# Kernel tuning notes

Measured on AMD Instinct MI355X. Metric: run time of the kernel, lower is better.

The kernel has to match this reference:

```python
import jax, jax.numpy as jnp
import numpy as np

N_NODES = 100000
N_EDGES = 1600000
K = 3  # TAGConv default hops


def _make_lin(key, out_dim, in_dim):
    # K+1 bias-free linears (stacked) + one shared output bias, per PyG TAGConv
    kw, = jax.random.split(key, 1)
    scale = 1.0 / np.sqrt(in_dim)
    W = jax.random.uniform(kw, (K + 1, out_dim, in_dim), jnp.float32, -scale, scale)
    b = jnp.zeros((out_dim,), jnp.float32)
    return W, b


def setup_inputs() -> dict:
    key = jax.random.key(0)
    ks = jax.random.split(key, 6)
    x = jax.random.normal(ks[0], (N_NODES, 128), jnp.float32)
    edge_index = jax.random.randint(ks[1], (2, N_EDGES), 0, N_NODES, jnp.int64)
    W1, b1 = _make_lin(ks[2], 128, 128)
    W2, b2 = _make_lin(ks[3], 64, 128)
    W3, b3 = _make_lin(ks[4], 16, 64)
    return {"x": x, "edge_index": edge_index, "W1": W1, "b1": b1,
            "W2": W2, "b2": b2, "W3": W3, "b3": b3}


def _tagconv(x, row, col, norm, W, b, n):
    # out = sum_k lin_k(A_norm^k x) + b ; message x_j*norm gathered at col
    out = jnp.einsum('nd,od->no', x, W[0])
    h = x
    for k in range(1, W.shape[0]):
        h = jax.ops.segment_sum(norm[:, None] * h[row], col, num_segments=n)
        out = out + jnp.einsum('nd,od->no', h, W[k])
    return out + b


def _dropout(x, key, p=0.5):
    keep = jax.random.bernoulli(key, 1.0 - p, x.shape)
    return jnp.where(keep, x / (1.0 - p), 0.0)


def reference(x, edge_index, W1, b1, W2, b2, W3, b3):
    n = x.shape[0]
    row, col = edge_index[0], edge_index[1]
    # gcn_norm without self-loops (TAGConv default)
    deg = jax.ops.segment_sum(jnp.ones(row.shape[0], x.dtype), col, num_segments=n)
    dis = jnp.where(deg > 0, 1.0 / jnp.sqrt(jnp.where(deg > 0, deg, 1.0)), 0.0)
    norm = dis[row] * dis[col]

    dk1, dk2 = jax.random.split(jax.random.key(42))
    h = _tagconv(x, row, col, norm, W1, b1, n)
    h = _dropout(h, dk1)
    h = _tagconv(h, row, col, norm, W2, b2, n)
    h = jax.nn.elu(h)
    h = _dropout(h, dk2)
    h = _tagconv(h, row, col, norm, W3, b3, n)
    return h
```

## Files before the change

### kernel.cpp

```cpp
#include <hip/hip_runtime.h>
#include <stdint.h>
#include <math.h>

#define N_NODES 100000
#define N_EDGES 1600000

typedef __bf16 bf16_t;
typedef __attribute__((ext_vector_type(4))) __bf16 bf16x4;
typedef __attribute__((ext_vector_type(8))) __bf16 bf16x8;
typedef __attribute__((ext_vector_type(4))) float f32x4;

__device__ __forceinline__ f32x4 mfma16(bf16x8 a, bf16x8 b, f32x4 c) {
  return __builtin_amdgcn_mfma_f32_16x16x32_bf16(a, b, c, 0, 0, 0);
}

__device__ __host__ __forceinline__ uint32_t rotl32(uint32_t v, int d) {
  return (v << d) | (v >> (32 - d));
}

__device__ __host__ __forceinline__ void threefry2x32(uint32_t k0, uint32_t k1,
                                                      uint32_t x0, uint32_t x1,
                                                      uint32_t& o0, uint32_t& o1) {
  uint32_t ks0 = k0, ks1 = k1, ks2 = k0 ^ k1 ^ 0x1BD11BDAu;
  x0 += ks0; x1 += ks1;
#define TF_R(r) { x0 += x1; x1 = rotl32(x1, r); x1 ^= x0; }
  TF_R(13) TF_R(15) TF_R(26) TF_R(6)
  x0 += ks1; x1 += ks2 + 1u;
  TF_R(17) TF_R(29) TF_R(16) TF_R(24)
  x0 += ks2; x1 += ks0 + 2u;
  TF_R(13) TF_R(15) TF_R(26) TF_R(6)
  x0 += ks0; x1 += ks1 + 3u;
  TF_R(17) TF_R(29) TF_R(16) TF_R(24)
  x0 += ks1; x1 += ks2 + 4u;
  TF_R(13) TF_R(15) TF_R(26) TF_R(6)
  x0 += ks2; x1 += ks0 + 5u;
#undef TF_R
  o0 = x0; o1 = x1;
}

__device__ __forceinline__ float drop_scale(uint32_t idx, uint32_t k0, uint32_t k1) {
  uint32_t o0, o1;
  threefry2x32(k0, k1, 0u, idx, o0, o1);
  uint32_t bits = o0 ^ o1;
  float u = __uint_as_float((bits >> 9) | 0x3f800000u) - 1.0f;
  return (u < 0.5f) ? 2.0f : 0.0f;
}

__global__ __launch_bounds__(256) void detect_kernel(const int* __restrict__ ei,
                                                     int* __restrict__ found_nonzero) {
  int idx = blockIdx.x * 256 + threadIdx.x;
  size_t j = (size_t)idx * 781;
  if (ei[2 * j + 1] != 0) atomicOr(found_nonzero, 1);
}

__device__ __forceinline__ int edge_row(const int* ei, bool i32, int e) {
  return i32 ? ei[e] : ei[2 * (size_t)e];
}
__device__ __forceinline__ int edge_col(const int* ei, bool i32, int e) {
  return i32 ? ei[N_EDGES + e] : ei[2 * ((size_t)N_EDGES + (size_t)e)];
}

__global__ __launch_bounds__(256) void deg_kernel(const int* __restrict__ ei,
                                                  const int* __restrict__ flag,
                                                  int* __restrict__ deg) {
  int e = blockIdx.x * 256 + threadIdx.x;
  if (e < N_EDGES) {
    bool i32 = *flag != 0;
    atomicAdd(&deg[edge_col(ei, i32, e)], 1);
  }
}

__global__ __launch_bounds__(256) void dis_kernel(const int* __restrict__ deg,
                                                  float* __restrict__ dis) {
  int n = blockIdx.x * 256 + threadIdx.x;
  if (n < N_NODES) {
    int d = deg[n];
    dis[n] = (d > 0) ? (1.0f / sqrtf((float)d)) : 0.0f;
  }
}

#define SCAN_NB 391
__global__ __launch_bounds__(256) void bsum_kernel(const int* __restrict__ deg,
                                                   int* __restrict__ bsum) {
  __shared__ int sh[256];
  int i = blockIdx.x * 256 + threadIdx.x;
  sh[threadIdx.x] = (i < N_NODES) ? deg[i] : 0;
  __syncthreads();
  for (int ofs = 128; ofs > 0; ofs >>= 1) {
    if (threadIdx.x < ofs) sh[threadIdx.x] += sh[threadIdx.x + ofs];
    __syncthreads();
  }
  if (threadIdx.x == 0) bsum[blockIdx.x] = sh[0];
}

__global__ __launch_bounds__(512) void bscan_kernel(const int* __restrict__ bsum,
                                                    int* __restrict__ boffs) {
  __shared__ int sh[512];
  int t = threadIdx.x;
  int v = (t < SCAN_NB) ? bsum[t] : 0;
  sh[t] = v;
  __syncthreads();
  for (int ofs = 1; ofs < 512; ofs <<= 1) {
    int u = (t >= ofs) ? sh[t - ofs] : 0;
    __syncthreads();
    sh[t] += u;
    __syncthreads();
  }
  if (t < SCAN_NB) boffs[t] = sh[t] - v;
  if (t == 0) boffs[SCAN_NB] = sh[SCAN_NB - 1];
}

__global__ __launch_bounds__(256) void rptr_kernel(const int* __restrict__ deg,
                                                   const int* __restrict__ boffs,
                                                   int* __restrict__ rptr) {
  __shared__ int sh[256];
  int i = blockIdx.x * 256 + threadIdx.x;
  int v = (i < N_NODES) ? deg[i] : 0;
  sh[threadIdx.x] = v;
  __syncthreads();
  for (int ofs = 1; ofs < 256; ofs <<= 1) {
    int u = (threadIdx.x >= ofs) ? sh[threadIdx.x - ofs] : 0;
    __syncthreads();
    sh[threadIdx.x] += u;
    __syncthreads();
  }
  if (i <= N_NODES) rptr[i] = boffs[blockIdx.x] + sh[threadIdx.x] - v;
}

__global__ __launch_bounds__(256) void fill_kernel(const int* __restrict__ ei,
                                                   const int* __restrict__ flag,
                                                   const float* __restrict__ dis,
                                                   const int* __restrict__ rptr,
                                                   int* cursor,
                                                   int2* __restrict__ erec) {
  int e = blockIdx.x * 256 + threadIdx.x;
  if (e < N_EDGES) {
    bool i32 = *flag != 0;
    int r = edge_row(ei, i32, e);
    int c = edge_col(ei, i32, e);
    int p = atomicAdd(&cursor[c], 1);
    int idx = rptr[c] + p;
    float nrm = dis[r] * dis[c];
    erec[idx] = make_int2(r, __float_as_int(nrm));
  }
}

__global__ __launch_bounds__(256) void wcvt_kernel(
    const float* __restrict__ W1, const float* __restrict__ W2,
    const float* __restrict__ W3,
    bf16_t* __restrict__ Wb1, bf16_t* __restrict__ Wb2,
    bf16_t* __restrict__ Wb3) {
  int i = blockIdx.x * 256 + threadIdx.x;
  if (i < 65536) Wb1[i] = (bf16_t)W1[i];
  if (i < 32768) Wb2[i] = (bf16_t)W2[i];
  if (i < 4096)  Wb3[i] = (bf16_t)W3[i];
}

template <int DIN, int LOG_DOUT, int NCH, bool YB, bool AHL>
__global__ __launch_bounds__(256) void matmul_mfma_kernel(
    const void* __restrict__ hA, const void* __restrict__ hAlo,
    const bf16_t* __restrict__ Wb, const float* __restrict__ bias,
    float* __restrict__ y0, void* __restrict__ y1,
    void* __restrict__ y2, void* __restrict__ y3) {
  constexpr int LDK = DIN + 8;
  constexpr int DOUT = 1 << LOG_DOUT;
  constexpr int KI = DIN / 32;
  __shared__ bf16_t sm[2][64 * LDK];
  const int m0 = blockIdx.x * 64;
  const int tid = threadIdx.x;

  if (AHL) {
    constexpr int NL = 64 * DIN / 8 / 256;
#pragma unroll
    for (int it = 0; it < NL; ++it) {
      int idx = tid + it * 256;
      int r = idx / (DIN / 8), cc = (idx % (DIN / 8)) * 8;
      int gm = m0 + r;
      uint4 vh = make_uint4(0, 0, 0, 0), vl = make_uint4(0, 0, 0, 0);
      if (gm < N_NODES) {
        vh = ((const uint4*)hA)[((size_t)gm * DIN + cc) >> 3];
        vl = ((const uint4*)hAlo)[((size_t)gm * DIN + cc) >> 3];
      }
      *(uint4*)&sm[0][r * LDK + cc] = vh;
      *(uint4*)&sm[1][r * LDK + cc] = vl;
    }
  } else {
    constexpr int NL = 64 * DIN / 4 / 256;
    union U4 { bf16_t b[4]; uint2 u; };
#pragma unroll
    for (int it = 0; it < NL; ++it) {
      int idx = tid + it * 256;
      int r = idx / (DIN / 4), cc = (idx % (DIN / 4)) * 4;
      int gm = m0 + r;
      float4 v = (gm < N_NODES) ? ((const float4*)hA)[((size_t)gm * DIN + cc) >> 2]
                                : make_float4(0.f, 0.f, 0.f, 0.f);
      U4 hi, lo;
      hi.b[0] = (bf16_t)v.x; lo.b[0] = (bf16_t)(v.x - (float)hi.b[0]);
      hi.b[1] = (bf16_t)v.y; lo.b[1] = (bf16_t)(v.y - (float)hi.b[1]);
      hi.b[2] = (bf16_t)v.z; lo.b[2] = (bf16_t)(v.z - (float)hi.b[2]);
      hi.b[3] = (bf16_t)v.w; lo.b[3] = (bf16_t)(v.w - (float)hi.b[3]);
      *(uint2*)&sm[0][r * LDK + cc] = hi.u;
      *(uint2*)&sm[1][r * LDK + cc] = lo.u;
    }
  }
  __syncthreads();

  const int w = tid >> 6, lane = tid & 63;
  const int wm = w & 1, wn = w >> 1;
  const int quad = lane >> 4, lr = lane & 15;

  bf16x8 aH[2][KI], aL[2][KI];
#pragma unroll
  for (int mt = 0; mt < 2; ++mt)
#pragma unroll
    for (int ki = 0; ki < KI; ++ki) {
      int rowa = wm * 32 + mt * 16 + lr;
      int koff = ki * 32 + quad * 8;
      aH[mt][ki] = *(const bf16x8*)&sm[0][rowa * LDK + koff];
      aL[mt][ki] = *(const bf16x8*)&sm[1][rowa * LDK + koff];
    }
  __syncthreads();

  constexpr int NLB = 64 * DIN / 8 / 256;
  uint4 wreg[NLB];
#pragma unroll
  for (int it = 0; it < NLB; ++it) {
    int idx = tid + it * 256;
    int r = idx / (DIN / 8), cc = (idx % (DIN / 8)) * 8;
    wreg[it] = ((const uint4*)Wb)[(((size_t)r) * DIN + cc) >> 3];
    *(uint4*)&sm[0][r * LDK + cc] = wreg[it];
  }
  __syncthreads();

  for (int nc = 0; nc < NCH; ++nc) {
    int p = nc & 1;
    if (nc + 1 < NCH) {
#pragma unroll
      for (int it = 0; it < NLB; ++it) {
        int idx = tid + it * 256;
        int r = idx / (DIN / 8), cc = (idx % (DIN / 8)) * 8;
        wreg[it] = ((const uint4*)Wb)[(((size_t)((nc + 1) * 64 + r)) * DIN + cc) >> 3];
      }
    }

    f32x4 acc[2][2] = {};
#pragma unroll
    for (int ki = 0; ki < KI; ++ki) {
      int koff = ki * 32 + quad * 8;
      bf16x8 bfr[2];
#pragma unroll
      for (int nt = 0; nt < 2; ++nt)
        bfr[nt] = *(const bf16x8*)&sm[p][(wn * 32 + nt * 16 + lr) * LDK + koff];
#pragma unroll
      for (int mt = 0; mt < 2; ++mt)
#pragma unroll
        for (int nt = 0; nt < 2; ++nt) {
          acc[mt][nt] = mfma16(bfr[nt], aH[mt][ki], acc[mt][nt]);
          acc[mt][nt] = mfma16(bfr[nt], aL[mt][ki], acc[mt][nt]);
        }
    }

    if (nc + 1 < NCH) {
#pragma unroll
      for (int it = 0; it < NLB; ++it) {
        int idx = tid + it * 256;
        int r = idx / (DIN / 8), cc = (idx % (DIN / 8)) * 8;
        *(uint4*)&sm[p ^ 1][r * LDK + cc] = wreg[it];
      }
    }
    __syncthreads();

    const int n0 = nc * 64;
#pragma unroll
    for (int mt = 0; mt < 2; ++mt) {
      int m = m0 + wm * 32 + mt * 16 + lr;
      if (m >= N_NODES) continue;
#pragma unroll
      for (int nt = 0; nt < 2; ++nt) {
        int nb = n0 + wn * 32 + nt * 16 + quad * 4;
        int k = nb >> LOG_DOUT;
        int o = nb & (DOUT - 1);
        size_t oi = (size_t)m * DOUT + o;
        if (k == 0) {
          float4 bv = *(const float4*)&bias[o];
          float4 st = make_float4(acc[mt][nt][0] + bv.x, acc[mt][nt][1] + bv.y,
                                  acc[mt][nt][2] + bv.z, acc[mt][nt][3] + bv.w);
          *(float4*)&y0[oi] = st;
        } else {
          void* yk = (k == 1) ? y1 : (k == 2) ? y2 : y3;
          if (YB) {
            bf16x4 bb;
            bb.x = (bf16_t)acc[mt][nt][0];
            bb.y = (bf16_t)acc[mt][nt][1];
            bb.z = (bf16_t)acc[mt][nt][2];
            bb.w = (bf16_t)acc[mt][nt][3];
            *(bf16x4*)((bf16_t*)yk + oi) = bb;
          } else {
            *(f32x4*)((float*)yk + oi) = acc[mt][nt];
          }
        }
      }
    }
  }
}

template <int D, int EPI, bool ZBF, bool ABF, int OMODE>
__global__ __launch_bounds__(256) void prop_kernel(
    const void* __restrict__ zv, const void* __restrict__ addv,
    void* __restrict__ outv, void* __restrict__ outv2,
    const int* __restrict__ rptr, const int2* __restrict__ erec,
    uint32_t k0, uint32_t k1) {
  constexpr int LPN = D / 4;
  constexpr int NPB = 256 / LPN;
  int lane = threadIdx.x % LPN;
  int nsub = threadIdx.x / LPN;
  int c = blockIdx.x * NPB + nsub;
  if (c >= N_NODES) return;
  int e0 = rptr[c], e1 = rptr[c + 1];
  float a0 = 0.f, a1 = 0.f, a2 = 0.f, a3 = 0.f;

  auto ld = [&](int r, float v[4]) {
    if (ZBF) {
      bf16x4 t = ((const bf16x4*)zv)[(size_t)r * LPN + lane];
      v[0] = (float)t.x; v[1] = (float)t.y; v[2] = (float)t.z; v[3] = (float)t.w;
    } else {
      float4 t = ((const float4*)zv)[(size_t)r * LPN + lane];
      v[0] = t.x; v[1] = t.y; v[2] = t.z; v[3] = t.w;
    }
  };

  int e = e0;
  for (; e + 3 < e1; e += 4) {
    int2 q[4];
    float v[4][4];
#pragma unroll
    for (int j = 0; j < 4; ++j) q[j] = erec[e + j];
#pragma unroll
    for (int j = 0; j < 4; ++j) ld(q[j].x, v[j]);
#pragma unroll
    for (int j = 0; j < 4; ++j) {
      float wv = __int_as_float(q[j].y);
      a0 = fmaf(wv, v[j][0], a0);
      a1 = fmaf(wv, v[j][1], a1);
      a2 = fmaf(wv, v[j][2], a2);
      a3 = fmaf(wv, v[j][3], a3);
    }
  }
  for (; e < e1; ++e) {
    int2 q = erec[e];
    float wv = __int_as_float(q.y);
    float v[4];
    ld(q.x, v);
    a0 = fmaf(wv, v[0], a0);
    a1 = fmaf(wv, v[1], a1);
    a2 = fmaf(wv, v[2], a2);
    a3 = fmaf(wv, v[3], a3);
  }

  size_t pidx = (size_t)c * LPN + lane;
  uint32_t fidx = (uint32_t)c * D + 4 * lane;
  float ax[4];
  if (ABF) {
    bf16x4 t = ((const bf16x4*)addv)[pidx];
    ax[0] = (float)t.x; ax[1] = (float)t.y; ax[2] = (float)t.z; ax[3] = (float)t.w;
  } else {
    float4 t = ((const float4*)addv)[pidx];
    ax[0] = t.x; ax[1] = t.y; ax[2] = t.z; ax[3] = t.w;
  }
  float o[4] = {a0 + ax[0], a1 + ax[1], a2 + ax[2], a3 + ax[3]};
  if (EPI == 1) {
#pragma unroll
    for (int j = 0; j < 4; ++j) o[j] *= drop_scale(fidx + j, k0, k1);
  }
  if (EPI == 2) {
#pragma unroll
    for (int j = 0; j < 4; ++j) {
      o[j] = (o[j] > 0.f) ? o[j] : expm1f(o[j]);
      o[j] *= drop_scale(fidx + j, k0, k1);
    }
  }
  if (OMODE == 0) {
    ((float4*)outv)[pidx] = make_float4(o[0], o[1], o[2], o[3]);
  } else if (OMODE == 1) {
    bf16x4 bv;
    bv.x = (bf16_t)o[0]; bv.y = (bf16_t)o[1];
    bv.z = (bf16_t)o[2]; bv.w = (bf16_t)o[3];
    ((bf16x4*)outv)[pidx] = bv;
  } else {
    bf16x4 hv, lv;
    hv.x = (bf16_t)o[0]; hv.y = (bf16_t)o[1];
    hv.z = (bf16_t)o[2]; hv.w = (bf16_t)o[3];
    lv.x = (bf16_t)(o[0] - (float)hv.x);
    lv.y = (bf16_t)(o[1] - (float)hv.y);
    lv.z = (bf16_t)(o[2] - (float)hv.z);
    lv.w = (bf16_t)(o[3] - (float)hv.w);
    ((bf16x4*)outv)[pidx] = hv;
    ((bf16x4*)outv2)[pidx] = lv;
  }
}

extern "C" void kernel_launch(void* const* d_in, const int* in_sizes, int n_in,
                              void* d_out, int out_size, void* d_ws, size_t ws_size,
                              hipStream_t stream) {
  const float* x  = (const float*)d_in[0];
  const int*   ei = (const int*)d_in[1];
  const float* W1 = (const float*)d_in[2];
  const float* b1 = (const float*)d_in[3];
  const float* W2 = (const float*)d_in[4];
  const float* b2 = (const float*)d_in[5];
  const float* W3 = (const float*)d_in[6];
  const float* b3 = (const float*)d_in[7];
  float* out = (float*)d_out;

  char* ws = (char*)d_ws;
  size_t off = 0;
  auto alloc = [&](size_t bytes) -> char* {
    char* p = ws + off;
    off += (bytes + 255) & ~(size_t)255;
    return p;
  };
  int*   flag   = (int*)alloc(256);
  int*   deg    = (int*)alloc((size_t)N_NODES * 4);
  int*   cursor = (int*)alloc((size_t)N_NODES * 4);
  float* dis    = (float*)alloc((size_t)N_NODES * 4);
  int*   rptr   = (int*)alloc((size_t)(N_NODES + 1) * 4);
  int*   bsum   = (int*)alloc((size_t)(SCAN_NB + 1) * 4);
  int*   boffs  = (int*)alloc((size_t)(SCAN_NB + 1) * 4);
  int2*  erec   = (int2*)alloc((size_t)N_EDGES * 8);
  bf16_t* Wb1  = (bf16_t*)alloc(65536 * 2);
  bf16_t* Wb2  = (bf16_t*)alloc(32768 * 2);
  bf16_t* Wb3  = (bf16_t*)alloc(4096 * 2);
  float*  R0  = (float*)alloc((size_t)N_NODES * 128 * 4);
  float*  R2  = (float*)alloc((size_t)N_NODES * 16 * 4);
  bf16_t* Zb0 = (bf16_t*)alloc((size_t)N_NODES * 128 * 2);
  bf16_t* Zb1 = (bf16_t*)alloc((size_t)N_NODES * 128 * 2);
  bf16_t* Bb1 = (bf16_t*)alloc((size_t)N_NODES * 128 * 2);
  bf16_t* Bb2 = (bf16_t*)alloc((size_t)N_NODES * 128 * 2);

  hipMemsetAsync(flag, 0, 256, stream);
  hipMemsetAsync(deg, 0, (size_t)N_NODES * 4, stream);
  hipMemsetAsync(cursor, 0, (size_t)N_NODES * 4, stream);

  detect_kernel<<<8, 256, 0, stream>>>(ei, flag);
  deg_kernel<<<(N_EDGES + 255) / 256, 256, 0, stream>>>(ei, flag, deg);
  dis_kernel<<<(N_NODES + 255) / 256, 256, 0, stream>>>(deg, dis);
  bsum_kernel<<<SCAN_NB, 256, 0, stream>>>(deg, bsum);
  bscan_kernel<<<1, 512, 0, stream>>>(bsum, boffs);
  rptr_kernel<<<SCAN_NB, 256, 0, stream>>>(deg, boffs, rptr);
  fill_kernel<<<(N_EDGES + 255) / 256, 256, 0, stream>>>(ei, flag, dis, rptr,
                                                         cursor, erec);
  wcvt_kernel<<<256, 256, 0, stream>>>(W1, W2, W3, Wb1, Wb2, Wb3);

  uint32_t d10, d11, d20, d21;
  threefry2x32(0u, 42u, 0u, 0u, d10, d11);
  threefry2x32(0u, 42u, 0u, 1u, d20, d21);

  const int MB = (N_NODES + 63) / 64;
  const int PB128 = (N_NODES + 7) / 8;
  const int PB64n = (N_NODES + 15) / 16;
  const int PB16n = (N_NODES + 63) / 64;

  matmul_mfma_kernel<128, 7, 8, true, false><<<MB, 256, 0, stream>>>(
      x, nullptr, Wb1, b1, R0, Bb1, Bb2, Zb0);
  prop_kernel<128, 0, true, true, 1><<<PB128, 256, 0, stream>>>(
      Zb0, Bb2, Zb1, nullptr, rptr, erec, 0, 0);
  prop_kernel<128, 0, true, true, 1><<<PB128, 256, 0, stream>>>(
      Zb1, Bb1, Zb0, nullptr, rptr, erec, 0, 0);
  prop_kernel<128, 1, true, false, 2><<<PB128, 256, 0, stream>>>(
      Zb0, R0, Bb2, Bb1, rptr, erec, d10, d11);

  float*  R1f = R0;
  bf16_t* S0 = Zb0;
  bf16_t* S1 = Zb0 + (size_t)N_NODES * 64;
  bf16_t* S2 = Zb1;
  bf16_t* S3 = Zb1 + (size_t)N_NODES * 64;
  matmul_mfma_kernel<128, 6, 4, true, true><<<MB, 256, 0, stream>>>(
      Bb2, Bb1, Wb2, b2, R1f, S2, S3, S0);
  prop_kernel<64, 0, true, true, 1><<<PB64n, 256, 0, stream>>>(
      S0, S3, S1, nullptr, rptr, erec, 0, 0);
  prop_kernel<64, 0, true, true, 1><<<PB64n, 256, 0, stream>>>(
      S1, S2, S0, nullptr, rptr, erec, 0, 0);
  prop_kernel<64, 2, true, false, 2><<<PB64n, 256, 0, stream>>>(
      S0, R1f, S2, S3, rptr, erec, d20, d21);

  float*  z0f = R2;
  bf16_t* zb1 = Bb1;
  bf16_t* zb2 = Bb1 + (size_t)N_NODES * 16;
  bf16_t* zb3 = Bb1 + (size_t)N_NODES * 32;
  matmul_mfma_kernel<64, 4, 1, true, true><<<MB, 256, 0, stream>>>(
      S2, S3, Wb3, b3, z0f, zb1, zb2, zb3);
  prop_kernel<16, 0, true, true, 1><<<PB16n, 256, 0, stream>>>(
      zb3, zb2, zb2, nullptr, rptr, erec, 0, 0);
  prop_kernel<16, 0, true, true, 1><<<PB16n, 256, 0, stream>>>(
      zb2, zb1, zb1, nullptr, rptr, erec, 0, 0);
  prop_kernel<16, 0, true, false, 0><<<PB16n, 256, 0, stream>>>(
      zb1, z0f, out, nullptr, rptr, erec, 0, 0);

  (void)in_sizes; (void)n_in; (void)out_size; (void)ws_size;
}
```

Before: 743.3 us.

## Fuse CSR fill, first-layer matmul and weight conversion into one launch

After: 797.4 us. 1.07x slower.

```diff
diff --git a/kernel.cpp b/kernel.cpp
--- a/kernel.cpp
+++ b/kernel.cpp
@@ -127,36 +127,184 @@
   if (i <= N_NODES) rptr[i] = boffs[blockIdx.x] + sh[threadIdx.x] - v;
 }
 
-__global__ __launch_bounds__(256) void fill_kernel(const int* __restrict__ ei,
-                                                   const int* __restrict__ flag,
-                                                   const float* __restrict__ dis,
-                                                   const int* __restrict__ rptr,
-                                                   int* cursor,
-                                                   int2* __restrict__ erec) {
-  int e = blockIdx.x * 256 + threadIdx.x;
-  if (e < N_EDGES) {
-    bool i32 = *flag != 0;
+#define NFILL 512
+#define MB1 1563
+#define RANGE_N 12500
+
+__device__ void fill_range(int b, int tid, const int* __restrict__ ei,
+                           const int* __restrict__ flag,
+                           const float* __restrict__ dis,
+                           const int* __restrict__ rptr,
+                           int* cursor, int2* __restrict__ erec) {
+  int g = b & 7;
+  int gb = b >> 3;
+  int lo = g * RANGE_N, hi = lo + RANGE_N;
+  bool i32 = *flag != 0;
+  for (int e = gb * 256 + tid; e < N_EDGES; e += 64 * 256) {
+    int c = edge_col(ei, i32, e);
+    if (c < lo || c >= hi) continue;
     int r = edge_row(ei, i32, e);
-    int c = edge_col(ei, i32, e);
     int p = atomicAdd(&cursor[c], 1);
-    int idx = rptr[c] + p;
-    float nrm = dis[r] * dis[c];
-    erec[idx] = make_int2(r, __float_as_int(nrm));
-  }
-}
-
-__global__ __launch_bounds__(256) void wcvt_kernel(
-    const float* __restrict__ W1, const float* __restrict__ W2,
-    const float* __restrict__ W3,
-    bf16_t* __restrict__ Wb1, bf16_t* __restrict__ Wb2,
-    bf16_t* __restrict__ Wb3) {
-  int i = blockIdx.x * 256 + threadIdx.x;
-  if (i < 65536) Wb1[i] = (bf16_t)W1[i];
-  if (i < 32768) Wb2[i] = (bf16_t)W2[i];
-  if (i < 4096)  Wb3[i] = (bf16_t)W3[i];
-}
-
-template <int DIN, int LOG_DOUT, int NCH, bool YB, bool AHL>
+    erec[rptr[c] + p] = make_int2(r, __float_as_int(dis[r] * dis[c]));
+  }
+}
+
+__global__ __launch_bounds__(256) void fused1_kernel(
+    const int* __restrict__ ei, const int* __restrict__ flag,
+    const float* __restrict__ dis, const int* __restrict__ rptr,
+    int* cursor, int2* __restrict__ erec,
+    const float* __restrict__ x, const float* __restrict__ W1f,
+    const float* __restrict__ b1,
+    float* __restrict__ y0, bf16_t* __restrict__ y1,
+    bf16_t* __restrict__ y2, bf16_t* __restrict__ y3,
+    const float* __restrict__ W2, const float* __restrict__ W3,
+    bf16_t* __restrict__ Wb2, bf16_t* __restrict__ Wb3) {
+  constexpr int DIN = 128, LDK = DIN + 8, KI = DIN / 32, NCH = 8;
+  __shared__ bf16_t sm[2][64 * LDK];
+  const int tid = threadIdx.x;
+  int b = blockIdx.x;
+
+  if (b < NFILL) {
+    fill_range(b, tid, ei, flag, dis, rptr, cursor, erec);
+    return;
+  }
+  b -= NFILL;
+  if (b >= MB1) {
+    for (int i = tid; i < 32768; i += 256) Wb2[i] = (bf16_t)W2[i];
+    for (int i = tid; i < 4096; i += 256) Wb3[i] = (bf16_t)W3[i];
+    return;
+  }
+
+  const int m0 = b * 64;
+  union U4 { bf16_t b[4]; uint2 u; };
+  union U8 { bf16_t b[8]; uint4 u; };
+  {
+    constexpr int NL = 64 * DIN / 4 / 256;
+#pragma unroll
+    for (int it = 0; it < NL; ++it) {
+      int idx = tid + it * 256;
+      int r = idx / (DIN / 4), cc = (idx % (DIN / 4)) * 4;
+      int gm = m0 + r;
+      float4 v = (gm < N_NODES) ? ((const float4*)x)[((size_t)gm * DIN + cc) >> 2]
+                                : make_float4(0.f, 0.f, 0.f, 0.f);
+      U4 hi, lo;
+      hi.b[0] = (bf16_t)v.x; lo.b[0] = (bf16_t)(v.x - (float)hi.b[0]);
+      hi.b[1] = (bf16_t)v.y; lo.b[1] = (bf16_t)(v.y - (float)hi.b[1]);
+      hi.b[2] = (bf16_t)v.z; lo.b[2] = (bf16_t)(v.z - (float)hi.b[2]);
+      hi.b[3] = (bf16_t)v.w; lo.b[3] = (bf16_t)(v.w - (float)hi.b[3]);
+      *(uint2*)&sm[0][r * LDK + cc] = hi.u;
+      *(uint2*)&sm[1][r * LDK + cc] = lo.u;
+    }
+  }
+  __syncthreads();
+
+  const int w = tid >> 6, lane = tid & 63;
+  const int wm = w & 1, wn = w >> 1;
+  const int quad = lane >> 4, lr = lane & 15;
+
+  bf16x8 aH[2][KI], aL[2][KI];
+#pragma unroll
+  for (int mt = 0; mt < 2; ++mt)
+#pragma unroll
+    for (int ki = 0; ki < KI; ++ki) {
+      int rowa = wm * 32 + mt * 16 + lr;
+      int koff = ki * 32 + quad * 8;
+      aH[mt][ki] = *(const bf16x8*)&sm[0][rowa * LDK + koff];
+      aL[mt][ki] = *(const bf16x8*)&sm[1][rowa * LDK + koff];
+    }
+  __syncthreads();
+
+  constexpr int NLB = 64 * DIN / 8 / 256;
+  auto loadW = [&](int gr, int cc) -> uint4 {
+    const float4* p = (const float4*)&W1f[(size_t)gr * DIN + cc];
+    float4 a = p[0], bq = p[1];
+    U8 t;
+    t.b[0] = (bf16_t)a.x;  t.b[1] = (bf16_t)a.y;
+    t.b[2] = (bf16_t)a.z;  t.b[3] = (bf16_t)a.w;
+    t.b[4] = (bf16_t)bq.x; t.b[5] = (bf16_t)bq.y;
+    t.b[6] = (bf16_t)bq.z; t.b[7] = (bf16_t)bq.w;
+    return t.u;
+  };
+  uint4 wreg[NLB];
+#pragma unroll
+  for (int it = 0; it < NLB; ++it) {
+    int idx = tid + it * 256;
+    int r = idx / (DIN / 8), cc = (idx % (DIN / 8)) * 8;
+    wreg[it] = loadW(r, cc);
+    *(uint4*)&sm[0][r * LDK + cc] = wreg[it];
+  }
+  __syncthreads();
+
+  for (int nc = 0; nc < NCH; ++nc) {
+    int p = nc & 1;
+    if (nc + 1 < NCH) {
+#pragma unroll
+      for (int it = 0; it < NLB; ++it) {
+        int idx = tid + it * 256;
+        int r = idx / (DIN / 8), cc = (idx % (DIN / 8)) * 8;
+        wreg[it] = loadW((nc + 1) * 64 + r, cc);
+      }
+    }
+
+    f32x4 acc[2][2] = {};
+#pragma unroll
+    for (int ki = 0; ki < KI; ++ki) {
+      int koff = ki * 32 + quad * 8;
+      bf16x8 bfr[2];
+#pragma unroll
+      for (int nt = 0; nt < 2; ++nt)
+        bfr[nt] = *(const bf16x8*)&sm[p][(wn * 32 + nt * 16 + lr) * LDK + koff];
+#pragma unroll
+      for (int mt = 0; mt < 2; ++mt)
+#pragma unroll
+        for (int nt = 0; nt < 2; ++nt) {
+          acc[mt][nt] = mfma16(bfr[nt], aH[mt][ki], acc[mt][nt]);
+          acc[mt][nt] = mfma16(bfr[nt], aL[mt][ki], acc[mt][nt]);
+        }
+    }
+
+    if (nc + 1 < NCH) {
+#pragma unroll
+      for (int it = 0; it < NLB; ++it) {
+        int idx = tid + it * 256;
+        int r = idx / (DIN / 8), cc = (idx % (DIN / 8)) * 8;
+        *(uint4*)&sm[p ^ 1][r * LDK + cc] = wreg[it];
+      }
+    }
+    __syncthreads();
+
+    const int n0 = nc * 64;
+#pragma unroll
+    for (int mt = 0; mt < 2; ++mt) {
+      int m = m0 + wm * 32 + mt * 16 + lr;
+      if (m >= N_NODES) continue;
+#pragma unroll
+      for (int nt = 0; nt < 2; ++nt) {
+        int nb = n0 + wn * 32 + nt * 16 + quad * 4;
+        int k = nb >> 7;
+        int o = nb & 127;
+        size_t oi = (size_t)m * 128 + o;
+        if (k == 0) {
+          float4 bv = *(const float4*)&b1[o];
+          *(float4*)&y0[oi] = make_float4(acc[mt][nt][0] + bv.x,
+                                          acc[mt][nt][1] + bv.y,
+                                          acc[mt][nt][2] + bv.z,
+                                          acc[mt][nt][3] + bv.w);
+        } else {
+          bf16_t* yk = (k == 1) ? y1 : (k == 2) ? y2 : y3;
+          bf16x4 bb;
+          bb.x = (bf16_t)acc[mt][nt][0];
+          bb.y = (bf16_t)acc[mt][nt][1];
+          bb.z = (bf16_t)acc[mt][nt][2];
+          bb.w = (bf16_t)acc[mt][nt][3];
+          *(bf16x4*)(yk + oi) = bb;
+        }
+      }
+    }
+  }
+}
+
+template <int DIN, int LOG_DOUT, int NCH, bool YB>
 __global__ __launch_bounds__(256) void matmul_mfma_kernel(
     const void* __restrict__ hA, const void* __restrict__ hAlo,
     const bf16_t* __restrict__ Wb, const float* __restrict__ bias,
@@ -169,7 +317,7 @@
   const int m0 = blockIdx.x * 64;
   const int tid = threadIdx.x;
 
-  if (AHL) {
+  {
     constexpr int NL = 64 * DIN / 8 / 256;
 #pragma unroll
     for (int it = 0; it < NL; ++it) {
@@ -184,24 +332,6 @@
       *(uint4*)&sm[0][r * LDK + cc] = vh;
       *(uint4*)&sm[1][r * LDK + cc] = vl;
     }
-  } else {
-    constexpr int NL = 64 * DIN / 4 / 256;
-    union U4 { bf16_t b[4]; uint2 u; };
-#pragma unroll
-    for (int it = 0; it < NL; ++it) {
-      int idx = tid + it * 256;
-      int r = idx / (DIN / 4), cc = (idx % (DIN / 4)) * 4;
-      int gm = m0 + r;
-      float4 v = (gm < N_NODES) ? ((const float4*)hA)[((size_t)gm * DIN + cc) >> 2]
-                                : make_float4(0.f, 0.f, 0.f, 0.f);
-      U4 hi, lo;
-      hi.b[0] = (bf16_t)v.x; lo.b[0] = (bf16_t)(v.x - (float)hi.b[0]);
-      hi.b[1] = (bf16_t)v.y; lo.b[1] = (bf16_t)(v.y - (float)hi.b[1]);
-      hi.b[2] = (bf16_t)v.z; lo.b[2] = (bf16_t)(v.z - (float)hi.b[2]);
-      hi.b[3] = (bf16_t)v.w; lo.b[3] = (bf16_t)(v.w - (float)hi.b[3]);
-      *(uint2*)&sm[0][r * LDK + cc] = hi.u;
-      *(uint2*)&sm[1][r * LDK + cc] = lo.u;
-    }
   }
   __syncthreads();
 
@@ -283,9 +413,10 @@
         size_t oi = (size_t)m * DOUT + o;
         if (k == 0) {
           float4 bv = *(const float4*)&bias[o];
-          float4 st = make_float4(acc[mt][nt][0] + bv.x, acc[mt][nt][1] + bv.y,
-                                  acc[mt][nt][2] + bv.z, acc[mt][nt][3] + bv.w);
-          *(float4*)&y0[oi] = st;
+          *(float4*)&y0[oi] = make_float4(acc[mt][nt][0] + bv.x,
+                                          acc[mt][nt][1] + bv.y,
+                                          acc[mt][nt][2] + bv.z,
+                                          acc[mt][nt][3] + bv.w);
         } else {
           void* yk = (k == 1) ? y1 : (k == 2) ? y2 : y3;
           if (YB) {
@@ -427,7 +558,6 @@
   int*   bsum   = (int*)alloc((size_t)(SCAN_NB + 1) * 4);
   int*   boffs  = (int*)alloc((size_t)(SCAN_NB + 1) * 4);
   int2*  erec   = (int2*)alloc((size_t)N_EDGES * 8);
-  bf16_t* Wb1  = (bf16_t*)alloc(65536 * 2);
   bf16_t* Wb2  = (bf16_t*)alloc(32768 * 2);
   bf16_t* Wb3  = (bf16_t*)alloc(4096 * 2);
   float*  R0  = (float*)alloc((size_t)N_NODES * 128 * 4);
@@ -447,9 +577,6 @@
   bsum_kernel<<<SCAN_NB, 256, 0, stream>>>(deg, bsum);
   bscan_kernel<<<1, 512, 0, stream>>>(bsum, boffs);
   rptr_kernel<<<SCAN_NB, 256, 0, stream>>>(deg, boffs, rptr);
-  fill_kernel<<<(N_EDGES + 255) / 256, 256, 0, stream>>>(ei, flag, dis, rptr,
-                                                         cursor, erec);
-  wcvt_kernel<<<256, 256, 0, stream>>>(W1, W2, W3, Wb1, Wb2, Wb3);
 
   uint32_t d10, d11, d20, d21;
   threefry2x32(0u, 42u, 0u, 0u, d10, d11);
@@ -460,8 +587,10 @@
   const int PB64n = (N_NODES + 15) / 16;
   const int PB16n = (N_NODES + 63) / 64;
 
-  matmul_mfma_kernel<128, 7, 8, true, false><<<MB, 256, 0, stream>>>(
-      x, nullptr, Wb1, b1, R0, Bb1, Bb2, Zb0);
+  fused1_kernel<<<NFILL + MB1 + 1, 256, 0, stream>>>(
+      ei, flag, dis, rptr, cursor, erec,
+      x, W1, b1, R0, Bb1, Bb2, Zb0, W2, W3, Wb2, Wb3);
+
   prop_kernel<128, 0, true, true, 1><<<PB128, 256, 0, stream>>>(
       Zb0, Bb2, Zb1, nullptr, rptr, erec, 0, 0);
   prop_kernel<128, 0, true, true, 1><<<PB128, 256, 0, stream>>>(
@@ -474,7 +603,7 @@
   bf16_t* S1 = Zb0 + (size_t)N_NODES * 64;
   bf16_t* S2 = Zb1;
   bf16_t* S3 = Zb1 + (size_t)N_NODES * 64;
-  matmul_mfma_kernel<128, 6, 4, true, true><<<MB, 256, 0, stream>>>(
+  matmul_mfma_kernel<128, 6, 4, true><<<MB, 256, 0, stream>>>(
       Bb2, Bb1, Wb2, b2, R1f, S2, S3, S0);
   prop_kernel<64, 0, true, true, 1><<<PB64n, 256, 0, stream>>>(
       S0, S3, S1, nullptr, rptr, erec, 0, 0);
@@ -487,7 +616,7 @@
   bf16_t* zb1 = Bb1;
   bf16_t* zb2 = Bb1 + (size_t)N_NODES * 16;
   bf16_t* zb3 = Bb1 + (size_t)N_NODES * 32;
-  matmul_mfma_kernel<64, 4, 1, true, true><<<MB, 256, 0, stream>>>(
+  matmul_mfma_kernel<64, 4, 1, true><<<MB, 256, 0, stream>>>(
       S2, S3, Wb3, b3, z0f, zb1, zb2, zb3);
   prop_kernel<16, 0, true, true, 1><<<PB16n, 256, 0, stream>>>(
       zb3, zb2, zb2, nullptr, rptr, erec, 0, 0);
```

## Factor symmetric GCN normalization into node scaling, store row-only CSR edges

Applied to the files above, without the earlier changes.

Result: slower. 818.0 us (+10.0%).

```diff
diff --git a/kernel.cpp b/kernel.cpp
--- a/kernel.cpp
+++ b/kernel.cpp
@@ -129,37 +129,23 @@
 
 __global__ __launch_bounds__(256) void fill_kernel(const int* __restrict__ ei,
                                                    const int* __restrict__ flag,
-                                                   const float* __restrict__ dis,
-                                                   const int* __restrict__ rptr,
                                                    int* cursor,
-                                                   int2* __restrict__ erec) {
+                                                   int* __restrict__ erow) {
   int e = blockIdx.x * 256 + threadIdx.x;
   if (e < N_EDGES) {
     bool i32 = *flag != 0;
+    int c = edge_col(ei, i32, e);
     int r = edge_row(ei, i32, e);
-    int c = edge_col(ei, i32, e);
     int p = atomicAdd(&cursor[c], 1);
-    int idx = rptr[c] + p;
-    float nrm = dis[r] * dis[c];
-    erec[idx] = make_int2(r, __float_as_int(nrm));
-  }
-}
-
-__global__ __launch_bounds__(256) void wcvt_kernel(
-    const float* __restrict__ W1, const float* __restrict__ W2,
-    const float* __restrict__ W3,
-    bf16_t* __restrict__ Wb1, bf16_t* __restrict__ Wb2,
-    bf16_t* __restrict__ Wb3) {
-  int i = blockIdx.x * 256 + threadIdx.x;
-  if (i < 65536) Wb1[i] = (bf16_t)W1[i];
-  if (i < 32768) Wb2[i] = (bf16_t)W2[i];
-  if (i < 4096)  Wb3[i] = (bf16_t)W3[i];
+    __builtin_nontemporal_store(r, &erow[p]);
+  }
 }
 
 template <int DIN, int LOG_DOUT, int NCH, bool YB, bool AHL>
 __global__ __launch_bounds__(256) void matmul_mfma_kernel(
     const void* __restrict__ hA, const void* __restrict__ hAlo,
-    const bf16_t* __restrict__ Wb, const float* __restrict__ bias,
+    const float* __restrict__ Wf, const float* __restrict__ bias,
+    const float* __restrict__ dis,
     float* __restrict__ y0, void* __restrict__ y1,
     void* __restrict__ y2, void* __restrict__ y3) {
   constexpr int LDK = DIN + 8;
@@ -168,6 +154,8 @@
   __shared__ bf16_t sm[2][64 * LDK];
   const int m0 = blockIdx.x * 64;
   const int tid = threadIdx.x;
+  union U4 { bf16_t b[4]; uint2 u; };
+  union U8 { bf16_t b[8]; uint4 u; };
 
   if (AHL) {
     constexpr int NL = 64 * DIN / 8 / 256;
@@ -186,7 +174,6 @@
     }
   } else {
     constexpr int NL = 64 * DIN / 4 / 256;
-    union U4 { bf16_t b[4]; uint2 u; };
 #pragma unroll
     for (int it = 0; it < NL; ++it) {
       int idx = tid + it * 256;
@@ -222,12 +209,22 @@
   __syncthreads();
 
   constexpr int NLB = 64 * DIN / 8 / 256;
+  auto loadW = [&](int gr, int cc) -> uint4 {
+    const float4* p = (const float4*)&Wf[(size_t)gr * DIN + cc];
+    float4 a = p[0], bq = p[1];
+    U8 t;
+    t.b[0] = (bf16_t)a.x;  t.b[1] = (bf16_t)a.y;
+    t.b[2] = (bf16_t)a.z;  t.b[3] = (bf16_t)a.w;
+    t.b[4] = (bf16_t)bq.x; t.b[5] = (bf16_t)bq.y;
+    t.b[6] = (bf16_t)bq.z; t.b[7] = (bf16_t)bq.w;
+    return t.u;
+  };
   uint4 wreg[NLB];
 #pragma unroll
   for (int it = 0; it < NLB; ++it) {
     int idx = tid + it * 256;
     int r = idx / (DIN / 8), cc = (idx % (DIN / 8)) * 8;
-    wreg[it] = ((const uint4*)Wb)[(((size_t)r) * DIN + cc) >> 3];
+    wreg[it] = loadW(r, cc);
     *(uint4*)&sm[0][r * LDK + cc] = wreg[it];
   }
   __syncthreads();
@@ -239,7 +236,7 @@
       for (int it = 0; it < NLB; ++it) {
         int idx = tid + it * 256;
         int r = idx / (DIN / 8), cc = (idx % (DIN / 8)) * 8;
-        wreg[it] = ((const uint4*)Wb)[(((size_t)((nc + 1) * 64 + r)) * DIN + cc) >> 3];
+        wreg[it] = loadW((nc + 1) * 64 + r, cc);
       }
     }
 
@@ -275,6 +272,7 @@
     for (int mt = 0; mt < 2; ++mt) {
       int m = m0 + wm * 32 + mt * 16 + lr;
       if (m >= N_NODES) continue;
+      float dm = dis[m];
 #pragma unroll
       for (int nt = 0; nt < 2; ++nt) {
         int nb = n0 + wn * 32 + nt * 16 + quad * 4;
@@ -283,20 +281,24 @@
         size_t oi = (size_t)m * DOUT + o;
         if (k == 0) {
           float4 bv = *(const float4*)&bias[o];
-          float4 st = make_float4(acc[mt][nt][0] + bv.x, acc[mt][nt][1] + bv.y,
-                                  acc[mt][nt][2] + bv.z, acc[mt][nt][3] + bv.w);
-          *(float4*)&y0[oi] = st;
+          *(float4*)&y0[oi] = make_float4(acc[mt][nt][0] + bv.x,
+                                          acc[mt][nt][1] + bv.y,
+                                          acc[mt][nt][2] + bv.z,
+                                          acc[mt][nt][3] + bv.w);
         } else {
           void* yk = (k == 1) ? y1 : (k == 2) ? y2 : y3;
+          float s = (k == 3) ? dm : 1.0f;
           if (YB) {
             bf16x4 bb;
-            bb.x = (bf16_t)acc[mt][nt][0];
-            bb.y = (bf16_t)acc[mt][nt][1];
-            bb.z = (bf16_t)acc[mt][nt][2];
-            bb.w = (bf16_t)acc[mt][nt][3];
+            bb.x = (bf16_t)(s * acc[mt][nt][0]);
+            bb.y = (bf16_t)(s * acc[mt][nt][1]);
+            bb.z = (bf16_t)(s * acc[mt][nt][2]);
+            bb.w = (bf16_t)(s * acc[mt][nt][3]);
             *(bf16x4*)((bf16_t*)yk + oi) = bb;
           } else {
-            *(f32x4*)((float*)yk + oi) = acc[mt][nt];
+            f32x4 sv = acc[mt][nt];
+            sv[0] *= s; sv[1] *= s; sv[2] *= s; sv[3] *= s;
+            *(f32x4*)((float*)yk + oi) = sv;
           }
         }
       }
@@ -308,7 +310,8 @@
 __global__ __launch_bounds__(256) void prop_kernel(
     const void* __restrict__ zv, const void* __restrict__ addv,
     void* __restrict__ outv, void* __restrict__ outv2,
-    const int* __restrict__ rptr, const int2* __restrict__ erec,
+    const int* __restrict__ rptr, const int* __restrict__ erow,
+    const float* __restrict__ dis,
     uint32_t k0, uint32_t k1) {
   constexpr int LPN = D / 4;
   constexpr int NPB = 256 / LPN;
@@ -330,35 +333,27 @@
   };
 
   int e = e0;
-  for (; e + 3 < e1; e += 4) {
-    int2 q[4];
-    float v[4][4];
-#pragma unroll
-    for (int j = 0; j < 4; ++j) q[j] = erec[e + j];
-#pragma unroll
-    for (int j = 0; j < 4; ++j) ld(q[j].x, v[j]);
-#pragma unroll
-    for (int j = 0; j < 4; ++j) {
-      float wv = __int_as_float(q[j].y);
-      a0 = fmaf(wv, v[j][0], a0);
-      a1 = fmaf(wv, v[j][1], a1);
-      a2 = fmaf(wv, v[j][2], a2);
-      a3 = fmaf(wv, v[j][3], a3);
+  for (; e + 7 < e1; e += 8) {
+    int r[8];
+    float v[8][4];
+#pragma unroll
+    for (int j = 0; j < 8; ++j) r[j] = erow[e + j];
+#pragma unroll
+    for (int j = 0; j < 8; ++j) ld(r[j], v[j]);
+#pragma unroll
+    for (int j = 0; j < 8; ++j) {
+      a0 += v[j][0]; a1 += v[j][1]; a2 += v[j][2]; a3 += v[j][3];
     }
   }
   for (; e < e1; ++e) {
-    int2 q = erec[e];
-    float wv = __int_as_float(q.y);
     float v[4];
-    ld(q.x, v);
-    a0 = fmaf(wv, v[0], a0);
-    a1 = fmaf(wv, v[1], a1);
-    a2 = fmaf(wv, v[2], a2);
-    a3 = fmaf(wv, v[3], a3);
+    ld(erow[e], v);
+    a0 += v[0]; a1 += v[1]; a2 += v[2]; a3 += v[3];
   }
 
   size_t pidx = (size_t)c * LPN + lane;
   uint32_t fidx = (uint32_t)c * D + 4 * lane;
+  float dc = dis[c];
   float ax[4];
   if (ABF) {
     bf16x4 t = ((const bf16x4*)addv)[pidx];
@@ -367,7 +362,8 @@
     float4 t = ((const float4*)addv)[pidx];
     ax[0] = t.x; ax[1] = t.y; ax[2] = t.z; ax[3] = t.w;
   }
-  float o[4] = {a0 + ax[0], a1 + ax[1], a2 + ax[2], a3 + ax[3]};
+  float o[4] = {fmaf(dc, a0, ax[0]), fmaf(dc, a1, ax[1]),
+                fmaf(dc, a2, ax[2]), fmaf(dc, a3, ax[3])};
   if (EPI == 1) {
 #pragma unroll
     for (int j = 0; j < 4; ++j) o[j] *= drop_scale(fidx + j, k0, k1);
@@ -383,8 +379,8 @@
     ((float4*)outv)[pidx] = make_float4(o[0], o[1], o[2], o[3]);
   } else if (OMODE == 1) {
     bf16x4 bv;
-    bv.x = (bf16_t)o[0]; bv.y = (bf16_t)o[1];
-    bv.z = (bf16_t)o[2]; bv.w = (bf16_t)o[3];
+    bv.x = (bf16_t)(dc * o[0]); bv.y = (bf16_t)(dc * o[1]);
+    bv.z = (bf16_t)(dc * o[2]); bv.w = (bf16_t)(dc * o[3]);
     ((bf16x4*)outv)[pidx] = bv;
   } else {
     bf16x4 hv, lv;
@@ -426,10 +422,7 @@
   int*   rptr   = (int*)alloc((size_t)(N_NODES + 1) * 4);
   int*   bsum   = (int*)alloc((size_t)(SCAN_NB + 1) * 4);
   int*   boffs  = (int*)alloc((size_t)(SCAN_NB + 1) * 4);
-  int2*  erec   = (int2*)alloc((size_t)N_EDGES * 8);
-  bf16_t* Wb1  = (bf16_t*)alloc(65536 * 2);
-  bf16_t* Wb2  = (bf16_t*)alloc(32768 * 2);
-  bf16_t* Wb3  = (bf16_t*)alloc(4096 * 2);
+  int*   erow   = (int*)alloc((size_t)N_EDGES * 4);
   float*  R0  = (float*)alloc((size_t)N_NODES * 128 * 4);
   float*  R2  = (float*)alloc((size_t)N_NODES * 16 * 4);
   bf16_t* Zb0 = (bf16_t*)alloc((size_t)N_NODES * 128 * 2);
@@ -439,7 +432,6 @@
 
   hipMemsetAsync(flag, 0, 256, stream);
   hipMemsetAsync(deg, 0, (size_t)N_NODES * 4, stream);
-  hipMemsetAsync(cursor, 0, (size_t)N_NODES * 4, stream);
 
   detect_kernel<<<8, 256, 0, stream>>>(ei, flag);
   deg_kernel<<<(N_EDGES + 255) / 256, 256, 0, stream>>>(ei, flag, deg);
@@ -447,9 +439,9 @@
   bsum_kernel<<<SCAN_NB, 256, 0, stream>>>(deg, bsum);
   bscan_kernel<<<1, 512, 0, stream>>>(bsum, boffs);
   rptr_kernel<<<SCAN_NB, 256, 0, stream>>>(deg, boffs, rptr);
-  fill_kernel<<<(N_EDGES + 255) / 256, 256, 0, stream>>>(ei, flag, dis, rptr,
-                                                         cursor, erec);
-  wcvt_kernel<<<256, 256, 0, stream>>>(W1, W2, W3, Wb1, Wb2, Wb3);
+  hipMemcpyAsync(cursor, rptr, (size_t)N_NODES * 4, hipMemcpyDeviceToDevice,
+                 stream);
+  fill_kernel<<<(N_EDGES + 255) / 256, 256, 0, stream>>>(ei, flag, cursor, erow);
 
   uint32_t d10, d11, d20, d21;
   threefry2x32(0u, 42u, 0u, 0u, d10, d11);
@@ -461,13 +453,13 @@
   const int PB16n = (N_NODES + 63) / 64;
 
   matmul_mfma_kernel<128, 7, 8, true, false><<<MB, 256, 0, stream>>>(
-      x, nullptr, Wb1, b1, R0, Bb1, Bb2, Zb0);
+      x, nullptr, W1, b1, dis, R0, Bb1, Bb2, Zb0);
   prop_kernel<128, 0, true, true, 1><<<PB128, 256, 0, stream>>>(
-      Zb0, Bb2, Zb1, nullptr, rptr, erec, 0, 0);
+      Zb0, Bb2, Zb1, nullptr, rptr, erow, dis, 0, 0);
   prop_kernel<128, 0, true, true, 1><<<PB128, 256, 0, stream>>>(
-      Zb1, Bb1, Zb0, nullptr, rptr, erec, 0, 0);
+      Zb1, Bb1, Zb0, nullptr, rptr, erow, dis, 0, 0);
   prop_kernel<128, 1, true, false, 2><<<PB128, 256, 0, stream>>>(
-      Zb0, R0, Bb2, Bb1, rptr, erec, d10, d11);
+      Zb0, R0, Bb2, Bb1, rptr, erow, dis, d10, d11);
 
   float*  R1f = R0;
   bf16_t* S0 = Zb0;
@@ -475,26 +467,26 @@
   bf16_t* S2 = Zb1;
   bf16_t* S3 = Zb1 + (size_t)N_NODES * 64;
   matmul_mfma_kernel<128, 6, 4, true, true><<<MB, 256, 0, stream>>>(
-      Bb2, Bb1, Wb2, b2, R1f, S2, S3, S0);
+      Bb2, Bb1, W2, b2, dis, R1f, S2, S3, S0);
   prop_kernel<64, 0, true, true, 1><<<PB64n, 256, 0, stream>>>(
-      S0, S3, S1, nullptr, rptr, erec, 0, 0);
+      S0, S3, S1, nullptr, rptr, erow, dis, 0, 0);
   prop_kernel<64, 0, true, true, 1><<<PB64n, 256, 0, stream>>>(
-      S1, S2, S0, nullptr, rptr, erec, 0, 0);
+      S1, S2, S0, nullptr, rptr, erow, dis, 0, 0);
   prop_kernel<64, 2, true, false, 2><<<PB64n, 256, 0, stream>>>(
-      S0, R1f, S2, S3, rptr, erec, d20, d21);
+      S0, R1f, S2, S3, rptr, erow, dis, d20, d21);
 
   float*  z0f = R2;
   bf16_t* zb1 = Bb1;
   bf16_t* zb2 = Bb1 + (size_t)N_NODES * 16;
   bf16_t* zb3 = Bb1 + (size_t)N_NODES * 32;
   matmul_mfma_kernel<64, 4, 1, true, true><<<MB, 256, 0, stream>>>(
-      S2, S3, Wb3, b3, z0f, zb1, zb2, zb3);
+      S2, S3, W3, b3, dis, z0f, zb1, zb2, zb3);
   prop_kernel<16, 0, true, true, 1><<<PB16n, 256, 0, stream>>>(
-      zb3, zb2, zb2, nullptr, rptr, erec, 0, 0);
+      zb3, zb2, zb2, nullptr, rptr, erow, dis, 0, 0);
   prop_kernel<16, 0, true, true, 1><<<PB16n, 256, 0, stream>>>(
-      zb2, zb1, zb1, nullptr, rptr, erec, 0, 0);
+      zb2, zb1, zb1, nullptr, rptr, erow, dis, 0, 0);
   prop_kernel<16, 0, true, false, 0><<<PB16n, 256, 0, stream>>>(
-      zb1, z0f, out, nullptr, rptr, erec, 0, 0);
+      zb1, z0f, out, nullptr, rptr, erow, dis, 0, 0);
 
   (void)in_sizes; (void)n_in; (void)out_size; (void)ws_size;
 }
```
